# Kernel tuning notes

Measured on AMD Instinct MI355X. Metric: run time of the kernel, lower is better.

The kernel has to match this reference:

```python
import jax, jax.numpy as jnp
import numpy as np

N_NODES = 50000
N_EDGES = 800000
IN_C, HID_C, OUT_C, N_CLASSES = 256, 128, 128, 6
N_GRAPHS = 256
BN_EPS = 1e-5


def setup_inputs() -> dict:
    key = jax.random.key(0)
    ks = jax.random.split(key, 24)
    inp = {
        "x": jax.random.normal(ks[0], (N_NODES, IN_C), dtype=jnp.float32),
        "edge_index": jax.random.randint(ks[1], (2, N_EDGES), 0, N_NODES, dtype=jnp.int64),
        "batch": jnp.sort(jax.random.randint(ks[2], (N_NODES,), 0, N_GRAPHS, dtype=jnp.int64)),
    }
    dims = [(IN_C, HID_C), (HID_C, HID_C), (HID_C, OUT_C)]
    k = 3
    for i, (ci, co) in enumerate(dims):
        scale = 1.0 / np.sqrt(ci)
        inp[f"W{i}"] = jax.random.uniform(ks[k], (ci, co), minval=-scale, maxval=scale); k += 1
        inp[f"b{i}"] = jax.random.uniform(ks[k], (co,), minval=-scale, maxval=scale); k += 1
        inp[f"g{i}"] = jax.random.uniform(ks[k], (co,), minval=0.5, maxval=1.5); k += 1
        inp[f"bt{i}"] = 0.1 * jax.random.normal(ks[k], (co,)); k += 1
        inp[f"m{i}"] = 0.1 * jax.random.normal(ks[k], (co,)); k += 1
        inp[f"v{i}"] = jax.random.uniform(ks[k], (co,), minval=0.5, maxval=1.5); k += 1
    scale = 1.0 / np.sqrt(OUT_C)
    inp["lin_W"] = jax.random.uniform(ks[k], (OUT_C, N_CLASSES), minval=-scale, maxval=scale); k += 1
    inp["lin_b"] = jax.random.uniform(ks[k], (N_CLASSES,), minval=-scale, maxval=scale)
    return inp


def gcn_conv(x, W, b, row, col, n):
    # PyG GCNConv: linear transform, add self-loops, symmetric degree norm, scatter-add
    h = x @ W  # [N, Co]
    loop = jnp.arange(n, dtype=row.dtype)
    r = jnp.concatenate([row, loop])
    c = jnp.concatenate([col, loop])
    deg = jax.ops.segment_sum(jnp.ones_like(c, dtype=h.dtype), c, num_segments=n)
    dinv = jax.lax.rsqrt(deg)  # deg >= 1 thanks to self-loops
    norm = dinv[r] * dinv[c]  # [E+N]
    msg = h[r] * norm[:, None]
    return jax.ops.segment_sum(msg, c, num_segments=n) + b


def batch_norm(x, g, bt, m, v):
    return (x - m) * jax.lax.rsqrt(v + BN_EPS) * g + bt


def reference(x, edge_index, batch,
              W0, b0, g0, bt0, m0, v0,
              W1, b1, g1, bt1, m1, v1,
              W2, b2, g2, bt2, m2, v2,
              lin_W, lin_b):
    row, col = edge_index[0], edge_index[1]
    n = x.shape[0]
    params = [(W0, b0, g0, bt0, m0, v0), (W1, b1, g1, bt1, m1, v1), (W2, b2, g2, bt2, m2, v2)]
    h = x
    for (W, b, g, bt, m, v) in params:
        h = gcn_conv(h, W, b, row, col, n)
        h = batch_norm(h, g, bt, m, v)
        h = jax.nn.relu(h)  # dropout is identity in eval mode
    # global mean pool over graphs
    sums = jax.ops.segment_sum(h, batch, num_segments=N_GRAPHS)
    cnts = jax.ops.segment_sum(jnp.ones((n,), dtype=h.dtype), batch, num_segments=N_GRAPHS)
    pooled = sums / jnp.maximum(cnts, 1.0)[:, None]
    return pooled @ lin_W + lin_b  # [N_GRAPHS, N_CLASSES]
```

## Files before the change

kernel.cpp:

```cpp
#include <hip/hip_runtime.h>
#include <hip/hip_bf16.h>

#define N_NODES   50000
#define N_EDGES   800000
#define IN_C      256
#define HID_C     128
#define N_GRAPHS  256
#define N_CLASSES 6
#define BN_EPS    1e-5f


using bf16x8 = __attribute__((ext_vector_type(8))) short;
using f32x4  = __attribute__((ext_vector_type(4))) float;

__device__ __forceinline__ ushort f2bf(float f) {
    union { float f; unsigned u; } v; v.f = f;
    unsigned r = v.u + 0x7fffu + ((v.u >> 16) & 1u);
    return (ushort)(r >> 16);
}
__device__ __forceinline__ float bflo(unsigned u) {
    union { unsigned u; float f; } v; v.u = u << 16; return v.f;
}
__device__ __forceinline__ float bfhi(unsigned u) {
    union { unsigned u; float f; } v; v.u = u & 0xffff0000u; return v.f;
}

__global__ void k_count_rank(const int* __restrict__ col, int* __restrict__ ecnt,
                             int* __restrict__ rank, int e) {
    int i0 = (blockIdx.x * blockDim.x + threadIdx.x) * 4;
    if (i0 + 3 < e) {
        int4 c = *reinterpret_cast<const int4*>(col + i0);
        int4 r;
        r.x = atomicAdd(&ecnt[c.x], 1);
        r.y = atomicAdd(&ecnt[c.y], 1);
        r.z = atomicAdd(&ecnt[c.z], 1);
        r.w = atomicAdd(&ecnt[c.w], 1);
        *reinterpret_cast<int4*>(rank + i0) = r;
    } else {
        for (int i = i0; i < e; ++i) rank[i] = atomicAdd(&ecnt[col[i]], 1);
    }
}

__global__ void k_scanA(const int* __restrict__ ecnt, int* __restrict__ row_ptr,
                        int* __restrict__ bsum, float* __restrict__ dinv, int n) {
    __shared__ int s[256];
    int t = threadIdx.x;
    int i = blockIdx.x * 256 + t;
    int v = (i < n) ? ecnt[i] : 0;
    if (i < n) dinv[i] = rsqrtf((float)(v + 1));
    s[t] = v;
    __syncthreads();
    for (int d = 1; d < 256; d <<= 1) {
        int add = (t >= d) ? s[t - d] : 0;
        __syncthreads();
        s[t] += add;
        __syncthreads();
    }
    if (i < n) row_ptr[i] = s[t];
    if (t == 255) bsum[blockIdx.x] = s[255];
}

__global__ void k_scanC(const int* __restrict__ ecnt, int* __restrict__ row_ptr,
                        const int* __restrict__ bsum, int nb, int n, int e) {
    __shared__ int s[256];
    int t = threadIdx.x;
    int v = (t < nb) ? bsum[t] : 0;
    s[t] = v;
    __syncthreads();
    for (int d = 1; d < 256; d <<= 1) {
        int add = (t >= d) ? s[t - d] : 0;
        __syncthreads();
        s[t] += add;
        __syncthreads();
    }
    int off = (blockIdx.x > 0) ? s[blockIdx.x - 1] : 0;
    int i = blockIdx.x * 256 + t;
    if (i < n) row_ptr[i] = row_ptr[i] - ecnt[i] + off;
    if (i == 0) row_ptr[n] = e;
}

__global__ void k_fill(const int* __restrict__ row, const int* __restrict__ col,
                       const int* __restrict__ row_ptr, const int* __restrict__ rank,
                       const float* __restrict__ dinv, int2* __restrict__ wedge, int e) {
    int i0 = (blockIdx.x * blockDim.x + threadIdx.x) * 4;
    if (i0 + 3 < e) {
        int4 c  = *reinterpret_cast<const int4*>(col + i0);
        int4 r  = *reinterpret_cast<const int4*>(row + i0);
        int4 rk = *reinterpret_cast<const int4*>(rank + i0);
        wedge[row_ptr[c.x] + rk.x] = make_int2(r.x, __float_as_int(dinv[r.x]));
        wedge[row_ptr[c.y] + rk.y] = make_int2(r.y, __float_as_int(dinv[r.y]));
        wedge[row_ptr[c.z] + rk.z] = make_int2(r.z, __float_as_int(dinv[r.z]));
        wedge[row_ptr[c.w] + rk.w] = make_int2(r.w, __float_as_int(dinv[r.w]));
    } else {
        for (int i = i0; i < e; ++i)
            wedge[row_ptr[col[i]] + rank[i]] = make_int2(row[i], __float_as_int(dinv[row[i]]));
    }
}

__global__ void k_prepWF(const float* __restrict__ W0, const float* __restrict__ W1,
                         const float* __restrict__ W2, ushort* __restrict__ Wt0,
                         ushort* __restrict__ Wt1, ushort* __restrict__ Wt2,
                         const float* __restrict__ b0, const float* __restrict__ g0,
                         const float* __restrict__ bt0, const float* __restrict__ m0,
                         const float* __restrict__ v0,
                         const float* __restrict__ b1, const float* __restrict__ g1,
                         const float* __restrict__ bt1, const float* __restrict__ m1,
                         const float* __restrict__ v1,
                         const float* __restrict__ b2, const float* __restrict__ g2,
                         const float* __restrict__ bt2, const float* __restrict__ m2,
                         const float* __restrict__ v2,
                         float* __restrict__ fA, float* __restrict__ fC,
                         int* __restrict__ ecnt, int n) {
    int t = blockIdx.x * blockDim.x + threadIdx.x;
    if (t < n) ecnt[t] = 0;
    const int NW0 = 128 * IN_C, NW1 = 128 * HID_C;
    if (t < NW0) {
        int co = t / IN_C, k = t % IN_C;
        Wt0[t] = f2bf(W0[(size_t)k * 128 + co]);
    } else if (t < NW0 + NW1) {
        int u = t - NW0;
        int co = u / HID_C, k = u % HID_C;
        Wt1[u] = f2bf(W1[(size_t)k * 128 + co]);
    } else if (t < NW0 + 2 * NW1) {
        int u = t - NW0 - NW1;
        int co = u / HID_C, k = u % HID_C;
        Wt2[u] = f2bf(W2[(size_t)k * 128 + co]);
    } else if (t < NW0 + 2 * NW1 + 3 * 128) {
        int u = t - NW0 - 2 * NW1;
        int layer = u >> 7, c = u & 127;
        const float *b_, *g_, *bt_, *m_, *v_;
        if (layer == 0)      { b_ = b0; g_ = g0; bt_ = bt0; m_ = m0; v_ = v0; }
        else if (layer == 1) { b_ = b1; g_ = g1; bt_ = bt1; m_ = m1; v_ = v1; }
        else                 { b_ = b2; g_ = g2; bt_ = bt2; m_ = m2; v_ = v2; }
        float A = g_[c] * rsqrtf(v_[c] + BN_EPS);
        fA[u] = A;
        fC[u] = (b_[c] - m_[c]) * A + bt_[c];
    }
}

template <int K, bool AFP32>
__global__ __launch_bounds__(256) void k_gemmbf(const void* __restrict__ Av,
                                                const ushort* __restrict__ Wt,
                                                ushort* __restrict__ Cbf, int M) {
    extern __shared__ char smem[];
    const int tid = threadIdx.x;
    constexpr int CPC = K / 8;
    constexpr int NCH = 128 * CPC;
    for (int c = tid; c < NCH; c += 256) {
        int col = c / CPC, kg = c % CPC;
        float4 v = *reinterpret_cast<const float4*>(Wt + (size_t)col * K + kg * 8);
        int dst = col * (K * 2) + ((kg * 16) ^ ((col & 7) << 4));
        *reinterpret_cast<float4*>(smem + dst) = v;
    }
    __syncthreads();

    const int wave = tid >> 6, lane = tid & 63;
    const int l15 = lane & 15, lg = lane >> 4;
    const int row = blockIdx.x * 64 + wave * 16 + l15;
    const bool rok = (row < M);

    f32x4 acc[8] = {};

#pragma unroll
    for (int ks = 0; ks < K / 32; ++ks) {
        bf16x8 a;
        if (AFP32) {
            const float* Ap = (const float*)Av + (size_t)row * K + ks * 32 + lg * 8;
            float4 f0, f1;
            if (rok) {
                f0 = *reinterpret_cast<const float4*>(Ap);
                f1 = *reinterpret_cast<const float4*>(Ap + 4);
            } else {
                f0 = make_float4(0, 0, 0, 0); f1 = f0;
            }
            a[0] = (short)f2bf(f0.x); a[1] = (short)f2bf(f0.y);
            a[2] = (short)f2bf(f0.z); a[3] = (short)f2bf(f0.w);
            a[4] = (short)f2bf(f1.x); a[5] = (short)f2bf(f1.y);
            a[6] = (short)f2bf(f1.z); a[7] = (short)f2bf(f1.w);
        } else {
            if (rok) {
                const ushort* Ap = (const ushort*)Av + (size_t)row * K + ks * 32 + lg * 8;
                a = *reinterpret_cast<const bf16x8*>(Ap);
            } else {
#pragma unroll
                for (int j = 0; j < 8; ++j) a[j] = 0;
            }
        }
#pragma unroll
        for (int cf = 0; cf < 8; ++cf) {
            int col = cf * 16 + l15;
            int off = col * (K * 2) + ((ks * 64 + lg * 16) ^ ((col & 7) << 4));
            bf16x8 b = *reinterpret_cast<const bf16x8*>(smem + off);
            acc[cf] = __builtin_amdgcn_mfma_f32_16x16x32_bf16(a, b, acc[cf], 0, 0, 0);
        }
    }

#pragma unroll
    for (int cf = 0; cf < 8; ++cf) {
        int col = cf * 16 + l15;
#pragma unroll
        for (int i = 0; i < 4; ++i) {
            int r = blockIdx.x * 64 + wave * 16 + lg * 4 + i;
            if (r < M) Cbf[(size_t)r * 128 + col] = f2bf(acc[cf][i]);
        }
    }
}

__global__ __launch_bounds__(256) void k_aggbf(const ushort* __restrict__ h,
                                               const int* __restrict__ row_ptr,
                                               const int2* __restrict__ wedge,
                                               const float* __restrict__ dinv,
                                               const float* __restrict__ fA,
                                               const float* __restrict__ fC,
                                               ushort* __restrict__ out, int n) {
    int wave = threadIdx.x >> 6, lane = threadIdx.x & 63;
    int vtx = blockIdx.x * 4 + wave;
    if (vtx >= n) return;
    int q = lane >> 4, l15 = lane & 15;
    int c0 = l15 * 8;
    int2 rp = *reinterpret_cast<const int2*>(row_ptr + vtx);
    int beg = rp.x, end = rp.y;

    float a0 = 0.f, a1 = 0.f, a2 = 0.f, a3 = 0.f;
    float a4 = 0.f, a5 = 0.f, a6 = 0.f, a7 = 0.f;
    for (int e = beg + q; e < end; e += 16) {
        int eB = e + 4, eC = e + 8, eD = e + 12;
        bool kB = eB < end, kC = eC < end, kD = eD < end;
        int2 wd0 = wedge[e];
        int2 wd1 = wedge[kB ? eB : e];
        int2 wd2 = wedge[kC ? eC : e];
        int2 wd3 = wedge[kD ? eD : e];
        float w0 = __int_as_float(wd0.y);
        float w1 = kB ? __int_as_float(wd1.y) : 0.f;
        float w2 = kC ? __int_as_float(wd2.y) : 0.f;
        float w3 = kD ? __int_as_float(wd3.y) : 0.f;
        uint4 u0 = *reinterpret_cast<const uint4*>(h + (size_t)wd0.x * 128 + c0);
        uint4 u1 = *reinterpret_cast<const uint4*>(h + (size_t)wd1.x * 128 + c0);
        uint4 u2 = *reinterpret_cast<const uint4*>(h + (size_t)wd2.x * 128 + c0);
        uint4 u3 = *reinterpret_cast<const uint4*>(h + (size_t)wd3.x * 128 + c0);
        a0 = fmaf(bflo(u0.x), w0, a0); a1 = fmaf(bfhi(u0.x), w0, a1);
        a2 = fmaf(bflo(u0.y), w0, a2); a3 = fmaf(bfhi(u0.y), w0, a3);
        a4 = fmaf(bflo(u0.z), w0, a4); a5 = fmaf(bfhi(u0.z), w0, a5);
        a6 = fmaf(bflo(u0.w), w0, a6); a7 = fmaf(bfhi(u0.w), w0, a7);
        a0 = fmaf(bflo(u1.x), w1, a0); a1 = fmaf(bfhi(u1.x), w1, a1);
        a2 = fmaf(bflo(u1.y), w1, a2); a3 = fmaf(bfhi(u1.y), w1, a3);
        a4 = fmaf(bflo(u1.z), w1, a4); a5 = fmaf(bfhi(u1.z), w1, a5);
        a6 = fmaf(bflo(u1.w), w1, a6); a7 = fmaf(bfhi(u1.w), w1, a7);
        a0 = fmaf(bflo(u2.x), w2, a0); a1 = fmaf(bfhi(u2.x), w2, a1);
        a2 = fmaf(bflo(u2.y), w2, a2); a3 = fmaf(bfhi(u2.y), w2, a3);
        a4 = fmaf(bflo(u2.z), w2, a4); a5 = fmaf(bfhi(u2.z), w2, a5);
        a6 = fmaf(bflo(u2.w), w2, a6); a7 = fmaf(bfhi(u2.w), w2, a7);
        a0 = fmaf(bflo(u3.x), w3, a0); a1 = fmaf(bfhi(u3.x), w3, a1);
        a2 = fmaf(bflo(u3.y), w3, a2); a3 = fmaf(bfhi(u3.y), w3, a3);
        a4 = fmaf(bflo(u3.z), w3, a4); a5 = fmaf(bfhi(u3.z), w3, a5);
        a6 = fmaf(bflo(u3.w), w3, a6); a7 = fmaf(bfhi(u3.w), w3, a7);
    }

    a0 += __shfl_xor(a0, 16); a0 += __shfl_xor(a0, 32);
    a1 += __shfl_xor(a1, 16); a1 += __shfl_xor(a1, 32);
    a2 += __shfl_xor(a2, 16); a2 += __shfl_xor(a2, 32);
    a3 += __shfl_xor(a3, 16); a3 += __shfl_xor(a3, 32);
    a4 += __shfl_xor(a4, 16); a4 += __shfl_xor(a4, 32);
    a5 += __shfl_xor(a5, 16); a5 += __shfl_xor(a5, 32);
    a6 += __shfl_xor(a6, 16); a6 += __shfl_xor(a6, 32);
    a7 += __shfl_xor(a7, 16); a7 += __shfl_xor(a7, 32);

    if (q == 0) {
        float dv = dinv[vtx];
        float dvv = dv * dv;
        uint4 us = *reinterpret_cast<const uint4*>(h + (size_t)vtx * 128 + c0);
        float4 A0 = *reinterpret_cast<const float4*>(fA + c0);
        float4 A1 = *reinterpret_cast<const float4*>(fA + c0 + 4);
        float4 C0 = *reinterpret_cast<const float4*>(fC + c0);
        float4 C1 = *reinterpret_cast<const float4*>(fC + c0 + 4);
        float v0 = fmaf(a0, dv * A0.x, fmaf(bflo(us.x), dvv * A0.x, C0.x));
        float v1 = fmaf(a1, dv * A0.y, fmaf(bfhi(us.x), dvv * A0.y, C0.y));
        float v2 = fmaf(a2, dv * A0.z, fmaf(bflo(us.y), dvv * A0.z, C0.z));
        float v3 = fmaf(a3, dv * A0.w, fmaf(bfhi(us.y), dvv * A0.w, C0.w));
        float v4 = fmaf(a4, dv * A1.x, fmaf(bflo(us.z), dvv * A1.x, C1.x));
        float v5 = fmaf(a5, dv * A1.y, fmaf(bfhi(us.z), dvv * A1.y, C1.y));
        float v6 = fmaf(a6, dv * A1.z, fmaf(bflo(us.w), dvv * A1.z, C1.z));
        float v7 = fmaf(a7, dv * A1.w, fmaf(bfhi(us.w), dvv * A1.w, C1.w));
        v0 = fmaxf(v0, 0.f); v1 = fmaxf(v1, 0.f); v2 = fmaxf(v2, 0.f); v3 = fmaxf(v3, 0.f);
        v4 = fmaxf(v4, 0.f); v5 = fmaxf(v5, 0.f); v6 = fmaxf(v6, 0.f); v7 = fmaxf(v7, 0.f);
        uint4 packed;
        packed.x = (unsigned)f2bf(v0) | ((unsigned)f2bf(v1) << 16);
        packed.y = (unsigned)f2bf(v2) | ((unsigned)f2bf(v3) << 16);
        packed.z = (unsigned)f2bf(v4) | ((unsigned)f2bf(v5) << 16);
        packed.w = (unsigned)f2bf(v6) | ((unsigned)f2bf(v7) << 16);
        *reinterpret_cast<uint4*>(out + (size_t)vtx * 128 + c0) = packed;
    }
}

__global__ __launch_bounds__(256) void k_poolfinal(const ushort* __restrict__ h,
                                                   const int* __restrict__ batch,
                                                   const float* __restrict__ lw,
                                                   const float* __restrict__ lb,
                                                   float* __restrict__ out, int n) {
    __shared__ float psum[4][128];
    __shared__ float pool[128];
    int g = blockIdx.x;
    int tid = threadIdx.x;
    int wave = tid >> 6, lane = tid & 63;
    int lo = 0, hi = n;
    while (lo < hi) { int m = (lo + hi) >> 1; if (batch[m] < g) lo = m + 1; else hi = m; }
    int a = lo;
    lo = 0; hi = n;
    int g1 = g + 1;
    while (lo < hi) { int m = (lo + hi) >> 1; if (batch[m] < g1) lo = m + 1; else hi = m; }
    int b = lo;

    int c0 = lane * 2;
    float a0 = 0.f, a1 = 0.f;
    int i = a + wave;
    for (; i + 12 < b; i += 16) {
        unsigned u0 = *reinterpret_cast<const unsigned*>(h + (size_t)i * 128 + c0);
        unsigned u1 = *reinterpret_cast<const unsigned*>(h + (size_t)(i + 4) * 128 + c0);
        unsigned u2 = *reinterpret_cast<const unsigned*>(h + (size_t)(i + 8) * 128 + c0);
        unsigned u3 = *reinterpret_cast<const unsigned*>(h + (size_t)(i + 12) * 128 + c0);
        a0 += bflo(u0) + bflo(u1) + bflo(u2) + bflo(u3);
        a1 += bfhi(u0) + bfhi(u1) + bfhi(u2) + bfhi(u3);
    }
    for (; i < b; i += 4) {
        unsigned u = *reinterpret_cast<const unsigned*>(h + (size_t)i * 128 + c0);
        a0 += bflo(u); a1 += bfhi(u);
    }
    psum[wave][c0] = a0;
    psum[wave][c0 + 1] = a1;
    __syncthreads();
    if (tid < 128) pool[tid] = psum[0][tid] + psum[1][tid] + psum[2][tid] + psum[3][tid];
    __syncthreads();
    if (tid < N_CLASSES) {
        float inv = 1.0f / fmaxf((float)(b - a), 1.0f);
        float s = 0.f;
        for (int k = 0; k < 128; ++k) s = fmaf(pool[k], lw[k * N_CLASSES + tid], s);
        out[g * N_CLASSES + tid] = s * inv + lb[tid];
    }
}

extern "C" void kernel_launch(void* const* d_in, const int* in_sizes, int n_in,
                              void* d_out, int out_size, void* d_ws, size_t ws_size,
                              hipStream_t stream) {
    const float* x      = (const float*)d_in[0];
    const int*   ei     = (const int*)d_in[1];
    const int*   batch  = (const int*)d_in[2];
    const float* W0  = (const float*)d_in[3];
    const float* b0  = (const float*)d_in[4];
    const float* g0  = (const float*)d_in[5];
    const float* bt0 = (const float*)d_in[6];
    const float* m0  = (const float*)d_in[7];
    const float* v0  = (const float*)d_in[8];
    const float* W1  = (const float*)d_in[9];
    const float* b1  = (const float*)d_in[10];
    const float* g1  = (const float*)d_in[11];
    const float* bt1 = (const float*)d_in[12];
    const float* m1  = (const float*)d_in[13];
    const float* v1  = (const float*)d_in[14];
    const float* W2  = (const float*)d_in[15];
    const float* b2  = (const float*)d_in[16];
    const float* g2  = (const float*)d_in[17];
    const float* bt2 = (const float*)d_in[18];
    const float* m2  = (const float*)d_in[19];
    const float* v2  = (const float*)d_in[20];
    const float* lw  = (const float*)d_in[21];
    const float* lb  = (const float*)d_in[22];
    float* out = (float*)d_out;

    const int N = in_sizes[2];
    const int E = in_sizes[1] / 2;
    const int* row = ei;
    const int* col = ei + E;

    char* ws = (char*)d_ws;
    size_t off = 0;
    auto alloc = [&](size_t bytes) {
        void* p = ws + off;
        off += (bytes + 511) & ~(size_t)511;
        return p;
    };
    ushort* hA     = (ushort*)alloc((size_t)N * 128 * 2);
    ushort* hB     = (ushort*)alloc((size_t)N * 128 * 2);
    ushort* Wt0    = (ushort*)alloc((size_t)128 * IN_C * 2);
    ushort* Wt1    = (ushort*)alloc((size_t)128 * HID_C * 2);
    ushort* Wt2    = (ushort*)alloc((size_t)128 * HID_C * 2);
    int*   ecnt    = (int*)alloc((size_t)N * 4);
    int*   rank    = (int*)alloc((size_t)E * 4);
    int*   row_ptr = (int*)alloc((size_t)(N + 1) * 4);
    int2*  wedge   = (int2*)alloc((size_t)E * 8);
    float* dinv    = (float*)alloc((size_t)N * 4);
    int*   bsum    = (int*)alloc(256 * 4);
    float* fA      = (float*)alloc(3 * 128 * 4);
    float* fC      = (float*)alloc(3 * 128 * 4);

    const int NB_n  = (N + 255) / 256;
    const int NB_e4 = (E / 4 + 255) / 256;

    const int PW = (128 * (IN_C + 2 * HID_C) + 3 * 128 + 255) / 256;
    k_prepWF<<<PW, 256, 0, stream>>>(W0, W1, W2, Wt0, Wt1, Wt2,
                                     b0, g0, bt0, m0, v0,
                                     b1, g1, bt1, m1, v1,
                                     b2, g2, bt2, m2, v2, fA, fC, ecnt, N);
    k_count_rank<<<NB_e4, 256, 0, stream>>>(col, ecnt, rank, E);
    k_scanA<<<NB_n, 256, 0, stream>>>(ecnt, row_ptr, bsum, dinv, N);
    k_scanC<<<NB_n, 256, 0, stream>>>(ecnt, row_ptr, bsum, NB_n, N, E);
    k_fill<<<NB_e4, 256, 0, stream>>>(row, col, row_ptr, rank, dinv, wedge, E);

    const int GB = (N + 63) / 64;
    const int AB = (N + 3) / 4;

    k_gemmbf<IN_C, true><<<GB, 256, IN_C * 128 * 2, stream>>>(x, Wt0, hB, N);
    k_aggbf<<<AB, 256, 0, stream>>>(hB, row_ptr, wedge, dinv, fA, fC, hA, N);
    k_gemmbf<HID_C, false><<<GB, 256, HID_C * 128 * 2, stream>>>(hA, Wt1, hB, N);
    k_aggbf<<<AB, 256, 0, stream>>>(hB, row_ptr, wedge, dinv, fA + 128, fC + 128, hA, N);
    k_gemmbf<HID_C, false><<<GB, 256, HID_C * 128 * 2, stream>>>(hA, Wt2, hB, N);
    k_aggbf<<<AB, 256, 0, stream>>>(hB, row_ptr, wedge, dinv, fA + 256, fC + 256, hA, N);

    k_poolfinal<<<N_GRAPHS, 256, 0, stream>>>(hA, batch, lw, lb, out, N);
}
```

Before: 225.3 us.

## Fuse edge degree counting into first GEMM via an extra atomic wave

The first-layer GEMM kernel gains a fifth wave per block that runs the edge in-degree counting and rank atomics, and the standalone count kernel is removed. The atomic-heavy counting is meant to overlap with the MFMA work of the first GEMM, saving a launch and its serialized runtime. The block size grows to 320 threads, which may change occupancy. The counting wave also waits at the shared-memory weight load barrier before starting.

```diff
diff --git a/kernel.cpp b/kernel.cpp
--- a/kernel.cpp
+++ b/kernel.cpp
@@ -23,22 +23,6 @@
 }
 __device__ __forceinline__ float bfhi(unsigned u) {
     union { unsigned u; float f; } v; v.u = u & 0xffff0000u; return v.f;
-}
-
-__global__ void k_count_rank(const int* __restrict__ col, int* __restrict__ ecnt,
-                             int* __restrict__ rank, int e) {
-    int i0 = (blockIdx.x * blockDim.x + threadIdx.x) * 4;
-    if (i0 + 3 < e) {
-        int4 c = *reinterpret_cast<const int4*>(col + i0);
-        int4 r;
-        r.x = atomicAdd(&ecnt[c.x], 1);
-        r.y = atomicAdd(&ecnt[c.y], 1);
-        r.z = atomicAdd(&ecnt[c.z], 1);
-        r.w = atomicAdd(&ecnt[c.w], 1);
-        *reinterpret_cast<int4*>(rank + i0) = r;
-    } else {
-        for (int i = i0; i < e; ++i) rank[i] = atomicAdd(&ecnt[col[i]], 1);
-    }
 }
 
 __global__ void k_scanA(const int* __restrict__ ecnt, int* __restrict__ row_ptr,
@@ -138,8 +122,90 @@
     }
 }
 
-template <int K, bool AFP32>
-__global__ __launch_bounds__(256) void k_gemmbf(const void* __restrict__ Av,
+__global__ __launch_bounds__(320) void k_gemm0_count(const float* __restrict__ Av,
+                                                     const ushort* __restrict__ Wt,
+                                                     ushort* __restrict__ Cbf, int M,
+                                                     const int* __restrict__ col,
+                                                     int* __restrict__ ecnt,
+                                                     int* __restrict__ rank,
+                                                     int E, int jiters) {
+    constexpr int K = IN_C;
+    extern __shared__ char smem[];
+    const int tid = threadIdx.x;
+    constexpr int CPC = K / 8;
+    constexpr int NCH = 128 * CPC;
+    for (int c = tid; c < NCH; c += 320) {
+        int col_ = c / CPC, kg = c % CPC;
+        float4 v = *reinterpret_cast<const float4*>(Wt + (size_t)col_ * K + kg * 8);
+        int dst = col_ * (K * 2) + ((kg * 16) ^ ((col_ & 7) << 4));
+        *reinterpret_cast<float4*>(smem + dst) = v;
+    }
+    __syncthreads();
+
+    if (tid >= 256) {
+        int lane = tid - 256;
+        int base = blockIdx.x * (jiters * 256);
+        for (int j = 0; j < jiters; ++j) {
+            int i0 = base + (j * 64 + lane) * 4;
+            if (i0 + 3 < E) {
+                int4 c4 = *reinterpret_cast<const int4*>(col + i0);
+                int4 r4;
+                r4.x = atomicAdd(&ecnt[c4.x], 1);
+                r4.y = atomicAdd(&ecnt[c4.y], 1);
+                r4.z = atomicAdd(&ecnt[c4.z], 1);
+                r4.w = atomicAdd(&ecnt[c4.w], 1);
+                *reinterpret_cast<int4*>(rank + i0) = r4;
+            } else {
+                for (int i = i0; i < E; ++i) rank[i] = atomicAdd(&ecnt[col[i]], 1);
+            }
+        }
+        return;
+    }
+
+    const int wave = tid >> 6, lane = tid & 63;
+    const int l15 = lane & 15, lg = lane >> 4;
+    const int row = blockIdx.x * 64 + wave * 16 + l15;
+    const bool rok = (row < M);
+
+    f32x4 acc[8] = {};
+
+#pragma unroll
+    for (int ks = 0; ks < K / 32; ++ks) {
+        bf16x8 a;
+        const float* Ap = Av + (size_t)row * K + ks * 32 + lg * 8;
+        float4 f0, f1;
+        if (rok) {
+            f0 = *reinterpret_cast<const float4*>(Ap);
+            f1 = *reinterpret_cast<const float4*>(Ap + 4);
+        } else {
+            f0 = make_float4(0, 0, 0, 0); f1 = f0;
+        }
+        a[0] = (short)f2bf(f0.x); a[1] = (short)f2bf(f0.y);
+        a[2] = (short)f2bf(f0.z); a[3] = (short)f2bf(f0.w);
+        a[4] = (short)f2bf(f1.x); a[5] = (short)f2bf(f1.y);
+        a[6] = (short)f2bf(f1.z); a[7] = (short)f2bf(f1.w);
+#pragma unroll
+        for (int cf = 0; cf < 8; ++cf) {
+            int c = cf * 16 + l15;
+            int off = c * (K * 2) + ((ks * 64 + lg * 16) ^ ((c & 7) << 4));
+            bf16x8 b = *reinterpret_cast<const bf16x8*>(smem + off);
+            acc[cf] = __builtin_amdgcn_mfma_f32_16x16x32_bf16(a, b, acc[cf], 0, 0, 0);
+        }
+    }
+
+#pragma unroll
+    for (int cf = 0; cf < 8; ++cf) {
+        int c = cf * 16 + l15;
+#pragma unroll
+        for (int i = 0; i < 4; ++i) {
+            int r = blockIdx.x * 64 + wave * 16 + lg * 4 + i;
+            if (r < M) Cbf[(size_t)r * 128 + c] = f2bf(acc[cf][i]);
+        }
+    }
+}
+
+template <int K>
+__global__ __launch_bounds__(256) void k_gemmbf(const ushort* __restrict__ Av,
                                                 const ushort* __restrict__ Wt,
                                                 ushort* __restrict__ Cbf, int M) {
     extern __shared__ char smem[];
@@ -164,27 +230,12 @@
 #pragma unroll
     for (int ks = 0; ks < K / 32; ++ks) {
         bf16x8 a;
-        if (AFP32) {
-            const float* Ap = (const float*)Av + (size_t)row * K + ks * 32 + lg * 8;
-            float4 f0, f1;
-            if (rok) {
-                f0 = *reinterpret_cast<const float4*>(Ap);
-                f1 = *reinterpret_cast<const float4*>(Ap + 4);
-            } else {
-                f0 = make_float4(0, 0, 0, 0); f1 = f0;
-            }
-            a[0] = (short)f2bf(f0.x); a[1] = (short)f2bf(f0.y);
-            a[2] = (short)f2bf(f0.z); a[3] = (short)f2bf(f0.w);
-            a[4] = (short)f2bf(f1.x); a[5] = (short)f2bf(f1.y);
-            a[6] = (short)f2bf(f1.z); a[7] = (short)f2bf(f1.w);
+        if (rok) {
+            const ushort* Ap = Av + (size_t)row * K + ks * 32 + lg * 8;
+            a = *reinterpret_cast<const bf16x8*>(Ap);
         } else {
-            if (rok) {
-                const ushort* Ap = (const ushort*)Av + (size_t)row * K + ks * 32 + lg * 8;
-                a = *reinterpret_cast<const bf16x8*>(Ap);
-            } else {
-#pragma unroll
-                for (int j = 0; j < 8; ++j) a[j] = 0;
-            }
+#pragma unroll
+            for (int j = 0; j < 8; ++j) a[j] = 0;
         }
 #pragma unroll
         for (int cf = 0; cf < 8; ++cf) {
@@ -394,25 +445,28 @@
 
     const int NB_n  = (N + 255) / 256;
     const int NB_e4 = (E / 4 + 255) / 256;
+    const int GB    = (N + 63) / 64;
+    const int AB    = (N + 3) / 4;
+
+    const int epb    = (E + GB - 1) / GB;
+    const int jiters = (epb + 255) / 256;
 
     const int PW = (128 * (IN_C + 2 * HID_C) + 3 * 128 + 255) / 256;
     k_prepWF<<<PW, 256, 0, stream>>>(W0, W1, W2, Wt0, Wt1, Wt2,
                                      b0, g0, bt0, m0, v0,
                                      b1, g1, bt1, m1, v1,
                                      b2, g2, bt2, m2, v2, fA, fC, ecnt, N);
-    k_count_rank<<<NB_e4, 256, 0, stream>>>(col, ecnt, rank, E);
+
+    k_gemm0_count<<<GB, 320, IN_C * 128 * 2, stream>>>(x, Wt0, hB, N,
+                                                       col, ecnt, rank, E, jiters);
     k_scanA<<<NB_n, 256, 0, stream>>>(ecnt, row_ptr, bsum, dinv, N);
     k_scanC<<<NB_n, 256, 0, stream>>>(ecnt, row_ptr, bsum, NB_n, N, E);
     k_fill<<<NB_e4, 256, 0, stream>>>(row, col, row_ptr, rank, dinv, wedge, E);
 
-    const int GB = (N + 63) / 64;
-    const int AB = (N + 3) / 4;
-
-    k_gemmbf<IN_C, true><<<GB, 256, IN_C * 128 * 2, stream>>>(x, Wt0, hB, N);
     k_aggbf<<<AB, 256, 0, stream>>>(hB, row_ptr, wedge, dinv, fA, fC, hA, N);
-    k_gemmbf<HID_C, false><<<GB, 256, HID_C * 128 * 2, stream>>>(hA, Wt1, hB, N);
+    k_gemmbf<HID_C><<<GB, 256, HID_C * 128 * 2, stream>>>(hA, Wt1, hB, N);
     k_aggbf<<<AB, 256, 0, stream>>>(hB, row_ptr, wedge, dinv, fA + 128, fC + 128, hA, N);
-    k_gemmbf<HID_C, false><<<GB, 256, HID_C * 128 * 2, stream>>>(hA, Wt2, hB, N);
+    k_gemmbf<HID_C><<<GB, 256, HID_C * 128 * 2, stream>>>(hA, Wt2, hB, N);
     k_aggbf<<<AB, 256, 0, stream>>>(hB, row_ptr, wedge, dinv, fA + 256, fC + 256, hA, N);
 
     k_poolfinal<<<N_GRAPHS, 256, 0, stream>>>(hA, batch, lw, lb, out, N);
```

New measurement: 209.9 us. -6.8%, faster.
